# Performance work log

Hardware: AMD Instinct MI355X
Metric: run time of the kernel (lower is better)

The kernel has to match this reference:

```python
import jax, jax.numpy as jnp
import numpy as np

B, N, C, H = 2, 384, 256, 4
D = C // H


def setup_inputs() -> dict:
    key = jax.random.key(0)
    k1, k2 = jax.random.split(key)
    x = jax.random.normal(k1, (B, N, C), dtype=jnp.float32)
    # nn.Linear(dim, 8*dim, bias=False) weight, scaled like default torch init magnitude
    W = jax.random.normal(k2, (8 * C, C), dtype=jnp.float32) / np.float32(np.sqrt(C))
    return {"x": x, "W": W}


def reference(x, W):
    Bx, Nx, Cx = x.shape
    Hh = H
    Dd = Cx // Hh
    scale = Dd ** -0.5
    # w(x): [B,N,8C] -> [B,N,8,H,D] -> [8,B,H,N,D]
    w = (x @ W.T).reshape(Bx, Nx, 8, Hh, Dd).transpose(2, 0, 3, 1, 4)
    a, b, c = w[0], w[1], w[2]          # w[3..5] (d,e,f) are unused in the torch forward
    v1, v2 = w[6], w[7]
    # pairwise logits, each [B,H,N,N]
    eAB = jnp.exp(jnp.einsum('bhid,bhjd->bhij', a, b) * scale)  # indexed [i,j]
    eCD = jnp.exp(jnp.einsum('bhid,bhjd->bhij', b, c) * scale)  # indexed [i,k]
    eEF = jnp.exp(jnp.einsum('bhid,bhjd->bhij', c, a) * scale)  # indexed [j,k]
    # exact factorization of exp(AB[ij]+CD[ik]+EF[jk]):
    # num[i,d] = sum_j eAB[ij] v1[jd] * (sum_k eCD[ik] eEF[jk] v2[kd])
    T = eEF[..., None] * v2[:, :, None, :, :]                   # [B,H,j,k,D]
    R = jnp.einsum('bhik,bhjkd->bhijd', eCD, T)                 # [B,H,i,j,D]
    num = jnp.einsum('bhij,bhjd,bhijd->bhid', eAB, v1, R)       # [B,H,N,D]
    den = jnp.sum(eAB * jnp.einsum('bhik,bhjk->bhij', eCD, eEF), axis=-1)  # [B,H,N]
    out = num / den[..., None]
    # [B,H,N,D] -> [B,N,H,D] -> [B,N,C]
    return out.transpose(0, 2, 1, 3).reshape(Bx, Nx, Cx)
```

## Files before the change

### kernel.cpp

```cpp
#include <hip/hip_runtime.h>
#include <math.h>

#define B_  2
#define N_  384
#define C_  256
#define H_  4
#define D_  64
#define NBH (B_*H_)
#define TSZ (NBH*N_*D_)
#define ESZ (NBH*N_*N_)
#define SCALE 0.125f
#define PIT 72
#define NWSLICE (NBH*N_*68)

typedef _Float16 f16;
typedef f16  f16x8 __attribute__((ext_vector_type(8)));
typedef f16  f16x4 __attribute__((ext_vector_type(4)));
typedef float f32x4 __attribute__((ext_vector_type(4)));

__global__ __launch_bounds__(256) void proj_kernel(const float* __restrict__ x,
                                                   const float* __restrict__ W,
                                                   float* __restrict__ proj) {
    __shared__ float Xs[32][68];
    __shared__ float Ws[32][68];
    const int tid = threadIdx.x;
    const int tx = tid & 15, ty = tid >> 4;
    const int m0 = blockIdx.x * 64;
    const int c0 = blockIdx.y * 64;
    const int t  = c0 >> 8;
    const int wbase = ((t >= 3) ? (t + 3) : t) * 256;

    float acc[4][4] = {{0.f}};
    for (int k0 = 0; k0 < 256; k0 += 32) {
        __syncthreads();
#pragma unroll
        for (int l = 0; l < 8; ++l) {
            const int idx = l * 256 + tid;
            const int mi = idx >> 5, kk = idx & 31;
            Xs[kk][mi] = x[(m0 + mi) * 256 + k0 + kk];
            const int rem = (c0 + mi) & 255;
            Ws[kk][mi] = W[(wbase + rem) * 256 + k0 + kk];
        }
        __syncthreads();
#pragma unroll
        for (int kk = 0; kk < 32; ++kk) {
            const float4 xf = *(const float4*)&Xs[kk][ty * 4];
            const float4 wf = *(const float4*)&Ws[kk][tx * 4];
            const float xa[4] = {xf.x, xf.y, xf.z, xf.w};
            const float wa[4] = {wf.x, wf.y, wf.z, wf.w};
#pragma unroll
            for (int q = 0; q < 4; ++q)
#pragma unroll
                for (int p = 0; p < 4; ++p)
                    acc[q][p] += xa[q] * wa[p];
        }
    }
#pragma unroll
    for (int q = 0; q < 4; ++q) {
        const int r = m0 + ty * 4 + q;
        const int b = r / N_;
        const int n = r - b * N_;
#pragma unroll
        for (int p = 0; p < 4; ++p) {
            const int rem = (c0 + tx * 4 + p) & 255;
            const int h = rem >> 6, d = rem & 63;
            proj[t * TSZ + ((b * H_ + h) * N_ + n) * D_ + d] = acc[q][p];
        }
    }
}

__global__ __launch_bounds__(256) void logits_kernel(const float* __restrict__ proj,
                                                     f16* __restrict__ eabt16,
                                                     float* __restrict__ ecd,
                                                     f16* __restrict__ eef16) {
    __shared__ float Xs[32][68];
    __shared__ float Ys[32][68];
    const int tid = threadIdx.x;
    const int tx = tid & 15, ty = tid >> 4;
    const int i0 = blockIdx.x * 64, j0 = blockIdx.y * 64;
    const int q  = blockIdx.z >> 3;
    const int bh = blockIdx.z & 7;
    const int xt = q;
    const int yt = (q == 2) ? 0 : (q + 1);
    const float* Xp = proj + xt * TSZ + bh * N_ * D_;
    const float* Yp = proj + yt * TSZ + bh * N_ * D_;

    float acc[4][4] = {{0.f}};
    for (int k0 = 0; k0 < 64; k0 += 32) {
        __syncthreads();
#pragma unroll
        for (int l = 0; l < 8; ++l) {
            const int idx = l * 256 + tid;
            const int mi = idx >> 5, kk = idx & 31;
            Xs[kk][mi] = Xp[(i0 + mi) * 64 + k0 + kk];
            Ys[kk][mi] = Yp[(j0 + mi) * 64 + k0 + kk];
        }
        __syncthreads();
#pragma unroll
        for (int kk = 0; kk < 32; ++kk) {
            const float4 xf = *(const float4*)&Xs[kk][ty * 4];
            const float4 yf = *(const float4*)&Ys[kk][tx * 4];
            const float xa[4] = {xf.x, xf.y, xf.z, xf.w};
            const float ya[4] = {yf.x, yf.y, yf.z, yf.w};
#pragma unroll
            for (int qq = 0; qq < 4; ++qq)
#pragma unroll
                for (int p = 0; p < 4; ++p)
                    acc[qq][p] += xa[qq] * ya[p];
        }
    }
#pragma unroll
    for (int qq = 0; qq < 4; ++qq)
#pragma unroll
        for (int p = 0; p < 4; ++p) {
            const float e = expf(acc[qq][p] * SCALE);
            const int ii = i0 + ty * 4 + qq;
            const int jj = j0 + tx * 4 + p;
            if (q == 0)      eabt16[(size_t)bh * N_ * N_ + jj * N_ + ii] = (f16)e;
            else if (q == 1) ecd   [(size_t)bh * N_ * N_ + ii * N_ + jj] = e;
            else             eef16 [(size_t)bh * N_ * N_ + ii * N_ + jj] = (f16)e;
        }
}

__global__ __launch_bounds__(256) void triplet_mfma_kernel(
        const f16*  __restrict__ eabt,
        const float* __restrict__ ecd,
        const f16*  __restrict__ eef,
        const float* __restrict__ v1,
        const float* __restrict__ v2,
        float* __restrict__ num0,
        float* __restrict__ num1) {
    __shared__ __align__(16) unsigned char smem_raw[25600];
    f16*   es   = (f16*)smem_raw;
    f16*   abts = es + 64 * PIT;
    float* v1s  = (float*)(smem_raw + 18432);
    float* v2k  = (float*)(smem_raw + 24576);

    const int tid  = threadIdx.x;
    const int lane = tid & 63;
    const int w    = tid >> 6;
    const int quad = lane >> 4;
    const int lr   = lane & 15;
    const int i0 = blockIdx.x * 64;
    const int dg = blockIdx.y;
    const int zz = blockIdx.z;
    const int bh    = zz & 7;
    const int split = zz >> 3;
    const int dd = dg * 4 + w;

    const f16*   eabtb = eabt + (size_t)bh * N_ * N_;
    const float* ecdb  = ecd  + (size_t)bh * N_ * N_;
    const f16*   eefb  = eef  + (size_t)bh * N_ * N_;
    const float* v1b   = v1 + (size_t)bh * N_ * D_;
    const float* v2b   = v2 + (size_t)bh * N_ * D_;
    float* numout = split ? num1 : num0;

#pragma unroll
    for (int it = 0; it < 6; ++it) {
        const int id = it * 256 + tid;
        const int j = id >> 2, c = id & 3;
        const int d2 = dg * 4 + c;
        v1s[id] = (d2 < 64) ? v1b[j * 64 + d2] : 1.0f;
    }

    float numacc[16];
#pragma unroll
    for (int r = 0; r < 16; ++r) numacc[r] = 0.f;

    const int ktbeg = split * 3;
    for (int kt = ktbeg; kt < ktbeg + 3; ++kt) {
        const int k0 = kt * 64;
        __syncthreads();
        {
            const int c = tid >> 6, k = tid & 63;
            const int d2 = dg * 4 + c;
            v2k[c * 64 + k] = (d2 < 64) ? v2b[(k0 + k) * 64 + d2] : 1.0f;
        }
        __syncthreads();
        float4 v2a[2][2];
#pragma unroll
        for (int ks = 0; ks < 2; ++ks) {
            v2a[ks][0] = *(const float4*)&v2k[w * 64 + ks * 32 + quad * 8];
            v2a[ks][1] = *(const float4*)&v2k[w * 64 + ks * 32 + quad * 8 + 4];
        }
        f16x8 af[4][2];
#pragma unroll
        for (int isub = 0; isub < 4; ++isub) {
            const float* rowp = ecdb + (i0 + isub * 16 + lr) * N_ + k0 + quad * 8;
#pragma unroll
            for (int ks = 0; ks < 2; ++ks) {
                const float4 c0 = *(const float4*)(rowp + ks * 32);
                const float4 c1 = *(const float4*)(rowp + ks * 32 + 4);
                union { f16 h[8]; f16x8 v; } pk;
                pk.h[0] = (f16)(c0.x * v2a[ks][0].x);
                pk.h[1] = (f16)(c0.y * v2a[ks][0].y);
                pk.h[2] = (f16)(c0.z * v2a[ks][0].z);
                pk.h[3] = (f16)(c0.w * v2a[ks][0].w);
                pk.h[4] = (f16)(c1.x * v2a[ks][1].x);
                pk.h[5] = (f16)(c1.y * v2a[ks][1].y);
                pk.h[6] = (f16)(c1.z * v2a[ks][1].z);
                pk.h[7] = (f16)(c1.w * v2a[ks][1].w);
                af[isub][ks] = pk.v;
            }
        }

        for (int jt = 0; jt < 6; ++jt) {
            const int j0 = jt * 64;
            __syncthreads();
#pragma unroll
            for (int it = 0; it < 2; ++it) {
                const int row = it * 32 + (tid >> 3);
                const int blk = tid & 7;
                *(uint4*)(es   + row * PIT + blk * 8) =
                    *(const uint4*)(eefb  + (j0 + row) * N_ + k0 + blk * 8);
                *(uint4*)(abts + row * PIT + blk * 8) =
                    *(const uint4*)(eabtb + (j0 + row) * N_ + i0 + blk * 8);
            }
            __syncthreads();
#pragma unroll
            for (int js = 0; js < 4; ++js) {
                const f16x8 bf0 = *(const f16x8*)(es + (js * 16 + lr) * PIT + quad * 8);
                const f16x8 bf1 = *(const f16x8*)(es + (js * 16 + lr) * PIT + (4 + quad) * 8);
                const float v1v = v1s[(j0 + js * 16 + lr) * 4 + w];
#pragma unroll
                for (int isub = 0; isub < 4; ++isub) {
                    f32x4 t = {0.f, 0.f, 0.f, 0.f};
                    t = __builtin_amdgcn_mfma_f32_16x16x32_f16(af[isub][0], bf0, t, 0, 0, 0);
                    t = __builtin_amdgcn_mfma_f32_16x16x32_f16(af[isub][1], bf1, t, 0, 0, 0);
                    const f16x4 ab = *(const f16x4*)(abts + (js * 16 + lr) * PIT +
                                                     isub * 16 + quad * 4);
#pragma unroll
                    for (int q = 0; q < 4; ++q)
                        numacc[isub * 4 + q] += (float)ab[q] * (v1v * t[q]);
                }
            }
        }
    }
#pragma unroll
    for (int r = 0; r < 16; ++r) {
        float v = numacc[r];
        v += __shfl_xor(v, 1);
        v += __shfl_xor(v, 2);
        v += __shfl_xor(v, 4);
        v += __shfl_xor(v, 8);
        numacc[r] = v;
    }
    if (lr == 0) {
#pragma unroll
        for (int r = 0; r < 16; ++r) {
            const int i = (r >> 2) * 16 + quad * 4 + (r & 3);
            numout[((size_t)bh * N_ + i0 + i) * 68 + dd] = numacc[r];
        }
    }
}

__global__ __launch_bounds__(256) void finalize_kernel(const float* __restrict__ num0,
                                                       const float* __restrict__ num1,
                                                       float* __restrict__ out) {
    const int o = blockIdx.x * 256 + threadIdx.x;
    const int b = o / (N_ * C_);
    const int rem = o - b * (N_ * C_);
    const int n = rem >> 8;
    const int cc = rem & 255;
    const int h = cc >> 6, d = cc & 63;
    const size_t base = (((size_t)b * H_ + h) * N_ + n) * 68;
    const float nmr = num0[base + d]  + num1[base + d];
    const float dnr = num0[base + 64] + num1[base + 64];
    out[o] = nmr / dnr;
}

extern "C" void kernel_launch(void* const* d_in, const int* in_sizes, int n_in,
                              void* d_out, int out_size, void* d_ws, size_t ws_size,
                              hipStream_t stream) {
    const float* x = (const float*)d_in[0];
    const float* W = (const float*)d_in[1];
    float* ws    = (float*)d_ws;
    float* proj  = ws;
    float* ecd   = ws + 5 * TSZ;
    float* num1  = ecd + ESZ;
    f16*   eabt  = (f16*)(num1 + NWSLICE);
    f16*   eef   = eabt + ESZ;
    float* num0  = ws;

    proj_kernel<<<dim3(12, 20), 256, 0, stream>>>(x, W, proj);
    logits_kernel<<<dim3(6, 6, 24), 256, 0, stream>>>(proj, eabt, ecd, eef);
    triplet_mfma_kernel<<<dim3(6, 17, 16), 256, 0, stream>>>(
        eabt, ecd, eef, proj + 3 * TSZ, proj + 4 * TSZ, num0, num1);
    finalize_kernel<<<dim3(768), 256, 0, stream>>>(num0, num1, (float*)d_out);
}
```

Measured before the change: 307.9 us.

## Stage ecd*v2 A-fragments in shared memory, prefetch eef tiles, read eabt directly

Builds the scaled ecd*v2 A-operand once per k-tile into a shared buffer laid out per d column, using coalesced float4 loads, instead of each wave gathering and converting its own strided global rows. The eef B-tile for the next j step is now loaded into registers while the current tile is computed, which overlaps global latency with MFMA work. The eabt tile is no longer staged in shared memory and is read straight from global or cache inside the inner loop. Shared memory per block roughly doubles, which can lower occupancy, and the direct eabt reads may add global latency to the inner loop.

```diff
diff --git a/kernel.cpp b/kernel.cpp
--- a/kernel.cpp
+++ b/kernel.cpp
@@ -130,11 +130,10 @@
         const float* __restrict__ v2,
         float* __restrict__ num0,
         float* __restrict__ num1) {
-    __shared__ __align__(16) unsigned char smem_raw[25600];
-    f16*   es   = (f16*)smem_raw;
-    f16*   abts = es + 64 * PIT;
-    float* v1s  = (float*)(smem_raw + 18432);
-    float* v2k  = (float*)(smem_raw + 24576);
+    __shared__ __align__(16) unsigned char smem_raw[52224];
+    f16*   us   = (f16*)smem_raw;
+    f16*   es   = us + 4 * 64 * PIT;
+    float* v1s  = (float*)(smem_raw + 46080);
 
     const int tid  = threadIdx.x;
     const int lane = tid & 63;
@@ -167,68 +166,75 @@
 #pragma unroll
     for (int r = 0; r < 16; ++r) numacc[r] = 0.f;
 
+    const f32x4 zero4 = {0.f, 0.f, 0.f, 0.f};
+
+    const int brow = tid >> 4;
+    const int kcol = (tid & 15) * 4;
+    const int srow = tid >> 3;
+    const int sblk = tid & 7;
+
     const int ktbeg = split * 3;
     for (int kt = ktbeg; kt < ktbeg + 3; ++kt) {
         const int k0 = kt * 64;
-        __syncthreads();
-        {
-            const int c = tid >> 6, k = tid & 63;
-            const int d2 = dg * 4 + c;
-            v2k[c * 64 + k] = (d2 < 64) ? v2b[(k0 + k) * 64 + d2] : 1.0f;
-        }
-        __syncthreads();
-        float4 v2a[2][2];
-#pragma unroll
-        for (int ks = 0; ks < 2; ++ks) {
-            v2a[ks][0] = *(const float4*)&v2k[w * 64 + ks * 32 + quad * 8];
-            v2a[ks][1] = *(const float4*)&v2k[w * 64 + ks * 32 + quad * 8 + 4];
-        }
+        float4 v2f[4];
+        if (dg < 16) {
+#pragma unroll
+            for (int e = 0; e < 4; ++e)
+                v2f[e] = *(const float4*)&v2b[(k0 + kcol + e) * 64 + dg * 4];
+        } else {
+#pragma unroll
+            for (int e = 0; e < 4; ++e)
+                v2f[e] = make_float4(1.f, 1.f, 1.f, 1.f);
+        }
+        __syncthreads();
+#pragma unroll
+        for (int it = 0; it < 4; ++it) {
+            const int row = it * 16 + brow;
+            const float4 c4 = *(const float4*)&ecdb[(i0 + row) * N_ + k0 + kcol];
+#pragma unroll
+            for (int d = 0; d < 4; ++d) {
+                union { f16 h[4]; unsigned long long u; } pk;
+                pk.h[0] = (f16)(c4.x * ((const float*)&v2f[0])[d]);
+                pk.h[1] = (f16)(c4.y * ((const float*)&v2f[1])[d]);
+                pk.h[2] = (f16)(c4.z * ((const float*)&v2f[2])[d]);
+                pk.h[3] = (f16)(c4.w * ((const float*)&v2f[3])[d]);
+                *(unsigned long long*)(us + d * 64 * PIT + row * PIT + kcol) = pk.u;
+            }
+        }
+        __syncthreads();
         f16x8 af[4][2];
 #pragma unroll
-        for (int isub = 0; isub < 4; ++isub) {
-            const float* rowp = ecdb + (i0 + isub * 16 + lr) * N_ + k0 + quad * 8;
-#pragma unroll
-            for (int ks = 0; ks < 2; ++ks) {
-                const float4 c0 = *(const float4*)(rowp + ks * 32);
-                const float4 c1 = *(const float4*)(rowp + ks * 32 + 4);
-                union { f16 h[8]; f16x8 v; } pk;
-                pk.h[0] = (f16)(c0.x * v2a[ks][0].x);
-                pk.h[1] = (f16)(c0.y * v2a[ks][0].y);
-                pk.h[2] = (f16)(c0.z * v2a[ks][0].z);
-                pk.h[3] = (f16)(c0.w * v2a[ks][0].w);
-                pk.h[4] = (f16)(c1.x * v2a[ks][1].x);
-                pk.h[5] = (f16)(c1.y * v2a[ks][1].y);
-                pk.h[6] = (f16)(c1.z * v2a[ks][1].z);
-                pk.h[7] = (f16)(c1.w * v2a[ks][1].w);
-                af[isub][ks] = pk.v;
-            }
-        }
+        for (int isub = 0; isub < 4; ++isub)
+#pragma unroll
+            for (int ks = 0; ks < 2; ++ks)
+                af[isub][ks] = *(const f16x8*)(us + w * 64 * PIT +
+                                               (isub * 16 + lr) * PIT + (ks * 4 + quad) * 8);
+
+        uint4 pf0 = *(const uint4*)(eefb + (srow) * N_ + k0 + sblk * 8);
+        uint4 pf1 = *(const uint4*)(eefb + (32 + srow) * N_ + k0 + sblk * 8);
 
         for (int jt = 0; jt < 6; ++jt) {
             const int j0 = jt * 64;
             __syncthreads();
-#pragma unroll
-            for (int it = 0; it < 2; ++it) {
-                const int row = it * 32 + (tid >> 3);
-                const int blk = tid & 7;
-                *(uint4*)(es   + row * PIT + blk * 8) =
-                    *(const uint4*)(eefb  + (j0 + row) * N_ + k0 + blk * 8);
-                *(uint4*)(abts + row * PIT + blk * 8) =
-                    *(const uint4*)(eabtb + (j0 + row) * N_ + i0 + blk * 8);
+            *(uint4*)(es + srow * PIT + sblk * 8)        = pf0;
+            *(uint4*)(es + (32 + srow) * PIT + sblk * 8) = pf1;
+            __syncthreads();
+            if (jt < 5) {
+                pf0 = *(const uint4*)(eefb + (j0 + 64 + srow) * N_ + k0 + sblk * 8);
+                pf1 = *(const uint4*)(eefb + (j0 + 96 + srow) * N_ + k0 + sblk * 8);
             }
-            __syncthreads();
 #pragma unroll
             for (int js = 0; js < 4; ++js) {
                 const f16x8 bf0 = *(const f16x8*)(es + (js * 16 + lr) * PIT + quad * 8);
                 const f16x8 bf1 = *(const f16x8*)(es + (js * 16 + lr) * PIT + (4 + quad) * 8);
                 const float v1v = v1s[(j0 + js * 16 + lr) * 4 + w];
+                const f16* abp = eabtb + (j0 + js * 16 + lr) * N_ + i0 + quad * 4;
 #pragma unroll
                 for (int isub = 0; isub < 4; ++isub) {
-                    f32x4 t = {0.f, 0.f, 0.f, 0.f};
-                    t = __builtin_amdgcn_mfma_f32_16x16x32_f16(af[isub][0], bf0, t, 0, 0, 0);
+                    f32x4 t;
+                    t = __builtin_amdgcn_mfma_f32_16x16x32_f16(af[isub][0], bf0, zero4, 0, 0, 0);
                     t = __builtin_amdgcn_mfma_f32_16x16x32_f16(af[isub][1], bf1, t, 0, 0, 0);
-                    const f16x4 ab = *(const f16x4*)(abts + (js * 16 + lr) * PIT +
-                                                     isub * 16 + quad * 4);
+                    const f16x4 ab = *(const f16x4*)(abp + isub * 16);
 #pragma unroll
                     for (int q = 0; q < 4; ++q)
                         numacc[isub * 4 + q] += (float)ab[q] * (v1v * t[q]);
```

Result: slower. 757.7 us (+146.1%).
